# Kernel tuning notes

Hardware: AMD Instinct MI355X
Metric: run time of the kernel (lower is better)

The kernel has to match this reference:

```python
import jax, jax.numpy as jnp
import numpy as np


def _gcn_layer(x, W, b, src, dst, n_nodes):
    # PyG GCNConv: add self-loops, symmetric normalization, then
    # out[i] = sum_j norm_ij * (x[j] @ W) + b, norm_ij = deg_i^-1/2 * deg_j^-1/2
    h = x @ W  # [N, F_out]
    deg = jax.ops.segment_sum(jnp.ones_like(dst, dtype=h.dtype), dst, num_segments=n_nodes)
    dinv = jnp.where(deg > 0, jax.lax.rsqrt(deg), 0.0)
    norm = dinv[src] * dinv[dst]  # [E_total]
    msg = h[src] * norm[:, None]  # [E_total, F_out]
    out = jax.ops.segment_sum(msg, dst, num_segments=n_nodes)
    return out + b


def _add_self_loops(edge_index, n_nodes):
    loops = jnp.arange(n_nodes, dtype=edge_index.dtype)
    src = jnp.concatenate([edge_index[0], loops])
    dst = jnp.concatenate([edge_index[1], loops])
    return src, dst


def setup_inputs() -> dict:
    key = jax.random.key(0)
    ks = jax.random.split(key, 4)
    N, E, DIN, DOUT = 50000, 800000, 128, 64
    HID = 2 * DOUT
    x = jax.random.normal(ks[0], (N, DIN), dtype=jnp.float32)
    edge_index = jax.random.randint(ks[1], (2, E), 0, N, dtype=jnp.int64)
    W1 = jax.random.normal(ks[2], (DIN, HID), dtype=jnp.float32) / np.sqrt(DIN)
    b1 = jnp.zeros((HID,), dtype=jnp.float32)
    W2 = jax.random.normal(ks[3], (HID, DOUT), dtype=jnp.float32) / np.sqrt(HID)
    b2 = jnp.zeros((DOUT,), dtype=jnp.float32)
    return {"x": x, "edge_index": edge_index, "W1": W1, "b1": b1, "W2": W2, "b2": b2}


def reference(x, edge_index, W1, b1, W2, b2):
    n_nodes = x.shape[0]
    src, dst = _add_self_loops(edge_index, n_nodes)
    h = jax.nn.relu(_gcn_layer(x, W1, b1, src, dst, n_nodes))
    h = jax.nn.relu(_gcn_layer(h, W2, b2, src, dst, n_nodes))
    return h
```

## Files before the change

kernel.cpp:

```cpp
#include <hip/hip_runtime.h>

#define F_DIN  128
#define F_HID  128
#define F_DOUT 64
#define CAP    64
#define CNT_S  16

typedef __bf16 bf16x8 __attribute__((ext_vector_type(8)));
typedef float f32x4 __attribute__((ext_vector_type(4)));
typedef unsigned short ushort8 __attribute__((ext_vector_type(8)));
typedef unsigned short ushort4v __attribute__((ext_vector_type(4)));
typedef unsigned int uint4v __attribute__((ext_vector_type(4)));
typedef unsigned int uint2v __attribute__((ext_vector_type(2)));

static __device__ __forceinline__ unsigned short f2bf(float f) {
  unsigned u = __builtin_bit_cast(unsigned, f);
  u += 0x7FFF + ((u >> 16) & 1);
  return (unsigned short)(u >> 16);
}
static __device__ __forceinline__ float bflo(unsigned u) {
  return __builtin_bit_cast(float, u << 16);
}
static __device__ __forceinline__ float bfhi(unsigned u) {
  return __builtin_bit_cast(float, u & 0xFFFF0000u);
}


__global__ __launch_bounds__(256) void prep_zero(const float* __restrict__ W1,
                                                 const float* __restrict__ W2,
                                                 unsigned short* __restrict__ Wt1,
                                                 unsigned short* __restrict__ Wt2,
                                                 uint4v* __restrict__ zbase, int n16) {
  int i = blockIdx.x * 256 + threadIdx.x;
  if (i < n16) zbase[i] = uint4v{0u, 0u, 0u, 0u};
  if (i < F_HID * F_DIN) {
    int c = i / F_DIN, k = i % F_DIN;
    Wt1[i] = f2bf(W1[k * F_HID + c]);
  }
  int j = i - F_HID * F_DIN;
  if (j >= 0 && j < F_DOUT * F_HID) {
    int c = j / F_HID, k = j % F_HID;
    Wt2[j] = f2bf(W2[k * F_DOUT + c]);
  }
}


__global__ __launch_bounds__(256) void degfill_kernel(const int* __restrict__ src,
                                                      const int* __restrict__ dst,
                                                      int* __restrict__ cnt,
                                                      unsigned short* __restrict__ csr,
                                                      int E, int PS) {
  const int pid = (int)blockIdx.x & 7;
  const int lo = pid * PS;
  const int nch = gridDim.x >> 3;
  int i = ((int)blockIdx.x >> 3) * 256 + threadIdx.x;
  const int stride = nch * 256;
  for (; i < E; i += stride) {
    int d = dst[i];
    if ((unsigned)(d - lo) < (unsigned)PS) {
      int r = atomicAdd(&cnt[d * CNT_S], 1);
      if (r < CAP) csr[d * CAP + r] = (unsigned short)src[i];
    }
  }
}


template <int BN, bool AF32>
static __device__ __forceinline__ void gemm_body(const void* __restrict__ Ap,
                                                 const unsigned short* __restrict__ Wt,
                                                 unsigned short* __restrict__ Cout,
                                                 int M, int bid, int tid) {
  constexpr int K = 128;
  constexpr int NT = BN / 16;
  const int wv = tid >> 6;
  const int lane = tid & 63;
  const int r = lane & 15, g = lane >> 4;
  const int r0 = bid * 128 + wv * 32;

  f32x4 acc[2][NT];
#pragma unroll
  for (int t = 0; t < 2; ++t)
#pragma unroll
    for (int c = 0; c < NT; ++c) acc[t][c] = f32x4{0.f, 0.f, 0.f, 0.f};

#pragma unroll
  for (int kk = 0; kk < 4; ++kk) {
    const int kbase = kk * 32 + g * 8;
    bf16x8 afrag[2];
#pragma unroll
    for (int t = 0; t < 2; ++t) {
      int row = r0 + t * 16 + r;
      if (row >= M) row = M - 1;
      if (AF32) {
        const float* ap = (const float*)Ap + (size_t)row * K + kbase;
        float4 f0 = *(const float4*)(ap);
        float4 f1 = *(const float4*)(ap + 4);
        ushort8 h;
        h[0] = f2bf(f0.x); h[1] = f2bf(f0.y); h[2] = f2bf(f0.z); h[3] = f2bf(f0.w);
        h[4] = f2bf(f1.x); h[5] = f2bf(f1.y); h[6] = f2bf(f1.z); h[7] = f2bf(f1.w);
        afrag[t] = __builtin_bit_cast(bf16x8, h);
      } else {
        const unsigned short* ap = (const unsigned short*)Ap + (size_t)row * K + kbase;
        uint4v u = *(const uint4v*)ap;
        afrag[t] = __builtin_bit_cast(bf16x8, u);
      }
    }
#pragma unroll
    for (int c = 0; c < NT; ++c) {
      const int col = c * 16 + r;
      uint4v ub = *(const uint4v*)(Wt + (size_t)col * K + kbase);
      bf16x8 bfrag = __builtin_bit_cast(bf16x8, ub);
      acc[0][c] = __builtin_amdgcn_mfma_f32_16x16x32_bf16(afrag[0], bfrag, acc[0][c], 0, 0, 0);
      acc[1][c] = __builtin_amdgcn_mfma_f32_16x16x32_bf16(afrag[1], bfrag, acc[1][c], 0, 0, 0);
    }
  }

#pragma unroll
  for (int t = 0; t < 2; ++t)
#pragma unroll
    for (int c = 0; c < NT; ++c) {
      const int col = c * 16 + r;
#pragma unroll
      for (int j = 0; j < 4; ++j) {
        int row = r0 + t * 16 + g * 4 + j;
        if (row < M) Cout[(size_t)row * BN + col] = f2bf(acc[t][c][j]);
      }
    }
}

__global__ __launch_bounds__(256) void fat_gemm1_dinv(const float* __restrict__ x,
                                                      const unsigned short* __restrict__ Wt1,
                                                      unsigned short* __restrict__ H1, int M,
                                                      const int* __restrict__ cnt,
                                                      float* __restrict__ dinv,
                                                      int N, int gemmBlocks) {
  const int b = (int)blockIdx.x;
  if (b < gemmBlocks) {
    gemm_body<F_HID, true>(x, Wt1, H1, M, b, threadIdx.x);
  } else {
    int i = (b - gemmBlocks) * 256 + threadIdx.x;
    if (i < N) {
      int deg = cnt[i * CNT_S];
      dinv[i] = rsqrtf((float)(deg + 1));
    }
  }
}


__global__ __launch_bounds__(256, 8) void agg128_gemm2(const unsigned short* __restrict__ H,
                                                       const int* __restrict__ cnt,
                                                       const unsigned short* __restrict__ csr,
                                                       const float* __restrict__ dinv,
                                                       const float* __restrict__ bias,
                                                       const unsigned short* __restrict__ Wt2,
                                                       unsigned short* __restrict__ H2,
                                                       int Nn) {
  const int tid = threadIdx.x;
  const int lane = tid & 63;
  const int wv = tid >> 6;
  const int q = lane >> 4, ql = lane & 15;
  const int lrow = wv * 4 + q;
  const int node = blockIdx.x * 16 + lrow;

  __shared__ unsigned short ldsa[16 * 136];

  unsigned words[4] = {0u, 0u, 0u, 0u};
  if (node < Nn) {
    const float di = dinv[node];
    int deg = cnt[node * CNT_S];
    const int degc = deg < CAP ? deg : CAP;
    const uint4v us = *(const uint4v*)(H + (size_t)node * 128 + ql * 8);
    const unsigned short* slab = csr + (size_t)node * CAP;

    float acc[8];
#pragma unroll
    for (int i = 0; i < 8; ++i) acc[i] = 0.f;

    for (int f0 = 0; f0 < degc; f0 += 4) {
      ushort4v pk = *(const ushort4v*)(slab + f0);
      int sidx[4];
      float w[4];
#pragma unroll
      for (int j = 0; j < 4; ++j) {
        int s = (int)pk[j];
        sidx[j] = s < Nn ? s : Nn - 1;
        w[j] = (f0 + j < degc) ? dinv[sidx[j]] : 0.f;
      }
      uint4v u[4];
#pragma unroll
      for (int j = 0; j < 4; ++j)
        u[j] = *(const uint4v*)(H + (size_t)sidx[j] * 128 + ql * 8);
#pragma unroll
      for (int j = 0; j < 4; ++j)
#pragma unroll
        for (int i = 0; i < 4; ++i) {
          acc[2 * i]     = fmaf(w[j], bflo(u[j][i]), acc[2 * i]);
          acc[2 * i + 1] = fmaf(w[j], bfhi(u[j][i]), acc[2 * i + 1]);
        }
    }

    const float di2 = di * di;
#pragma unroll
    for (int i = 0; i < 4; ++i) {
      float v0 = di * acc[2 * i]     + di2 * bflo(us[i]) + bias[ql * 8 + 2 * i];
      float v1 = di * acc[2 * i + 1] + di2 * bfhi(us[i]) + bias[ql * 8 + 2 * i + 1];
      v0 = fmaxf(v0, 0.f); v1 = fmaxf(v1, 0.f);
      words[i] = (unsigned)f2bf(v0) | ((unsigned)f2bf(v1) << 16);
    }
  }
  {
    uint4v o; o[0] = words[0]; o[1] = words[1]; o[2] = words[2]; o[3] = words[3];
    *(uint4v*)(&ldsa[lrow * 136 + ql * 8]) = o;
  }
  __syncthreads();

  const int r = lane & 15, g = lane >> 4;
  f32x4 c = f32x4{0.f, 0.f, 0.f, 0.f};
#pragma unroll
  for (int kk = 0; kk < 4; ++kk) {
    const int kbase = kk * 32 + g * 8;
    bf16x8 a = __builtin_bit_cast(bf16x8, *(const uint4v*)(&ldsa[r * 136 + kbase]));
    bf16x8 b = __builtin_bit_cast(bf16x8, *(const uint4v*)(Wt2 + (size_t)(wv * 16 + r) * 128 + kbase));
    c = __builtin_amdgcn_mfma_f32_16x16x32_bf16(a, b, c, 0, 0, 0);
  }
#pragma unroll
  for (int j = 0; j < 4; ++j) {
    int no = blockIdx.x * 16 + g * 4 + j;
    if (no < Nn) H2[(size_t)no * 64 + wv * 16 + r] = f2bf(c[j]);
  }
}

__global__ __launch_bounds__(256, 8) void agg64_kernel(const unsigned short* __restrict__ H,
                                                       const int* __restrict__ cnt,
                                                       const unsigned short* __restrict__ csr,
                                                       const float* __restrict__ dinv,
                                                       const float* __restrict__ bias,
                                                       float* __restrict__ out,
                                                       int Nn) {
  const int lane = threadIdx.x & 63;
  const int wv = threadIdx.x >> 6;
  const int q = lane >> 4, ql = lane & 15;
  const int node = blockIdx.x * 16 + wv * 4 + q;
  if (node >= Nn) return;

  const float di = dinv[node];
  int deg = cnt[node * CNT_S];
  const int degc = deg < CAP ? deg : CAP;
  const uint2v us = *(const uint2v*)(H + (size_t)node * 64 + ql * 4);
  const unsigned short* slab = csr + (size_t)node * CAP;

  float acc[4];
#pragma unroll
  for (int i = 0; i < 4; ++i) acc[i] = 0.f;

  for (int f0 = 0; f0 < degc; f0 += 4) {
    ushort4v pk = *(const ushort4v*)(slab + f0);
    int sidx[4];
    float w[4];
#pragma unroll
    for (int j = 0; j < 4; ++j) {
      int s = (int)pk[j];
      sidx[j] = s < Nn ? s : Nn - 1;
      w[j] = (f0 + j < degc) ? dinv[sidx[j]] : 0.f;
    }
    uint2v u[4];
#pragma unroll
    for (int j = 0; j < 4; ++j)
      u[j] = *(const uint2v*)(H + (size_t)sidx[j] * 64 + ql * 4);
#pragma unroll
    for (int j = 0; j < 4; ++j)
#pragma unroll
      for (int i = 0; i < 2; ++i) {
        acc[2 * i]     = fmaf(w[j], bflo(u[j][i]), acc[2 * i]);
        acc[2 * i + 1] = fmaf(w[j], bfhi(u[j][i]), acc[2 * i + 1]);
      }
  }

  const float di2 = di * di;
  float4 o;
  o.x = fmaxf(di * acc[0] + di2 * bflo(us[0]) + bias[ql * 4 + 0], 0.f);
  o.y = fmaxf(di * acc[1] + di2 * bfhi(us[0]) + bias[ql * 4 + 1], 0.f);
  o.z = fmaxf(di * acc[2] + di2 * bflo(us[1]) + bias[ql * 4 + 2], 0.f);
  o.w = fmaxf(di * acc[3] + di2 * bfhi(us[1]) + bias[ql * 4 + 3], 0.f);
  *(float4*)(out + (size_t)node * 64 + ql * 4) = o;
}


extern "C" void kernel_launch(void* const* d_in, const int* in_sizes, int n_in,
                              void* d_out, int out_size, void* d_ws, size_t ws_size,
                              hipStream_t stream) {
  const float* x  = (const float*)d_in[0];
  const int*   ei = (const int*)d_in[1];
  const float* W1 = (const float*)d_in[2];
  const float* b1 = (const float*)d_in[3];
  const float* W2 = (const float*)d_in[4];
  const float* b2 = (const float*)d_in[5];
  float* out = (float*)d_out;

  const int E = in_sizes[1] / 2;
  const int N = in_sizes[0] / F_DIN;
  const int* src = ei;
  const int* dst = ei + E;

  char* ws = (char*)d_ws;
  auto alloc = [&](size_t bytes) {
    char* p = ws;
    ws += (bytes + 255) & ~(size_t)255;
    return p;
  };
  int*            cnt  = (int*)alloc((size_t)N * CNT_S * 4);
  float*          dinv = (float*)alloc((size_t)N * 4);
  unsigned short* csr  = (unsigned short*)alloc((size_t)N * CAP * 2);
  unsigned short* H1   = (unsigned short*)alloc((size_t)N * F_HID * 2);
  unsigned short* H2   = (unsigned short*)alloc((size_t)N * F_DOUT * 2);
  unsigned short* Wt1  = (unsigned short*)alloc((size_t)F_HID * F_DIN * 2);
  unsigned short* Wt2  = (unsigned short*)alloc((size_t)F_DOUT * F_HID * 2);

  const int gb = (N + 127) / 128;
  const int nb = (N + 255) / 256;
  const int PS = (N + 7) / 8;
  const int zero16 = (N * CNT_S * 4) / 16;
  int pgrid = (zero16 + 255) / 256;
  const int wgrid = (F_HID * F_DIN + F_DOUT * F_HID + 255) / 256;
  if (pgrid < wgrid) pgrid = wgrid;

  prep_zero<<<pgrid, 256, 0, stream>>>(W1, W2, Wt1, Wt2, (uint4v*)cnt, zero16);

  degfill_kernel<<<2048, 256, 0, stream>>>(src, dst, cnt, csr, E, PS);

  fat_gemm1_dinv<<<gb + nb, 256, 0, stream>>>(x, Wt1, H1, N, cnt, dinv, N, gb);

  agg128_gemm2<<<(N + 15) / 16, 256, 0, stream>>>(H1, cnt, csr, dinv, b1, Wt2, H2, N);

  agg64_kernel<<<(N + 15) / 16, 256, 0, stream>>>(H2, cnt, csr, dinv, b2, out, N);
}
```

Before: 114.6 us.

## Store hidden features in column-sliced layout and split aggregation by column block

GEMM1 now writes H1 as eight 16-column slabs (N×16 each), and GEMM2 writes H2 as eight 8-column slabs. The aggregation kernels run one column slab per block, interleaved across blocks, so each gathered row segment is small and the working set per slab (1.6 MB or 0.8 MB) can stay in cache. The fused agg128+gemm2 kernel is split into a standalone aggregation, an extra out1 buffer and a separate gemm2 launch. The cost is an extra kernel launch, an out1 round trip through memory, and rereading the CSR indices and dinv values once per column block.

```diff
diff --git a/kernel.cpp b/kernel.cpp
--- a/kernel.cpp
+++ b/kernel.cpp
@@ -65,11 +65,11 @@
 }
 
 
-template <int BN, bool AF32>
+template <int BN, int MODE>
 static __device__ __forceinline__ void gemm_body(const void* __restrict__ Ap,
                                                  const unsigned short* __restrict__ Wt,
                                                  unsigned short* __restrict__ Cout,
-                                                 int M, int bid, int tid) {
+                                                 int M, int Nn, int bid, int tid) {
   constexpr int K = 128;
   constexpr int NT = BN / 16;
   const int wv = tid >> 6;
@@ -91,7 +91,7 @@
     for (int t = 0; t < 2; ++t) {
       int row = r0 + t * 16 + r;
       if (row >= M) row = M - 1;
-      if (AF32) {
+      if (MODE == 0) {
         const float* ap = (const float*)Ap + (size_t)row * K + kbase;
         float4 f0 = *(const float4*)(ap);
         float4 f1 = *(const float4*)(ap + 4);
@@ -100,7 +100,8 @@
         h[4] = f2bf(f1.x); h[5] = f2bf(f1.y); h[6] = f2bf(f1.z); h[7] = f2bf(f1.w);
         afrag[t] = __builtin_bit_cast(bf16x8, h);
       } else {
-        const unsigned short* ap = (const unsigned short*)Ap + (size_t)row * K + kbase;
+        const unsigned short* ap = (const unsigned short*)Ap +
+            (size_t)(kk * 2 + (g >> 1)) * ((size_t)Nn * 16) + (size_t)row * 16 + (g & 1) * 8;
         uint4v u = *(const uint4v*)ap;
         afrag[t] = __builtin_bit_cast(bf16x8, u);
       }
@@ -123,7 +124,12 @@
 #pragma unroll
       for (int j = 0; j < 4; ++j) {
         int row = r0 + t * 16 + g * 4 + j;
-        if (row < M) Cout[(size_t)row * BN + col] = f2bf(acc[t][c][j]);
+        if (row < M) {
+          if (MODE == 0)
+            Cout[(size_t)c * ((size_t)Nn * 16) + (size_t)row * 16 + r] = f2bf(acc[t][c][j]);
+          else
+            Cout[(size_t)(col >> 3) * ((size_t)Nn * 8) + (size_t)row * 8 + (col & 7)] = f2bf(acc[t][c][j]);
+        }
       }
     }
 }
@@ -136,7 +142,7 @@
                                                       int N, int gemmBlocks) {
   const int b = (int)blockIdx.x;
   if (b < gemmBlocks) {
-    gemm_body<F_HID, true>(x, Wt1, H1, M, b, threadIdx.x);
+    gemm_body<F_HID, 0>(x, Wt1, H1, M, N, b, threadIdx.x);
   } else {
     int i = (b - gemmBlocks) * 256 + threadIdx.x;
     if (i < N) {
@@ -146,143 +152,119 @@
   }
 }
 
-
-__global__ __launch_bounds__(256, 8) void agg128_gemm2(const unsigned short* __restrict__ H,
-                                                       const int* __restrict__ cnt,
-                                                       const unsigned short* __restrict__ csr,
-                                                       const float* __restrict__ dinv,
-                                                       const float* __restrict__ bias,
-                                                       const unsigned short* __restrict__ Wt2,
-                                                       unsigned short* __restrict__ H2,
-                                                       int Nn) {
-  const int tid = threadIdx.x;
-  const int lane = tid & 63;
-  const int wv = tid >> 6;
-  const int q = lane >> 4, ql = lane & 15;
-  const int lrow = wv * 4 + q;
-  const int node = blockIdx.x * 16 + lrow;
-
-  __shared__ unsigned short ldsa[16 * 136];
-
-  unsigned words[4] = {0u, 0u, 0u, 0u};
-  if (node < Nn) {
-    const float di = dinv[node];
-    int deg = cnt[node * CNT_S];
-    const int degc = deg < CAP ? deg : CAP;
-    const uint4v us = *(const uint4v*)(H + (size_t)node * 128 + ql * 8);
-    const unsigned short* slab = csr + (size_t)node * CAP;
-
-    float acc[8];
-#pragma unroll
-    for (int i = 0; i < 8; ++i) acc[i] = 0.f;
-
-    for (int f0 = 0; f0 < degc; f0 += 4) {
-      ushort4v pk = *(const ushort4v*)(slab + f0);
-      int sidx[4];
-      float w[4];
-#pragma unroll
-      for (int j = 0; j < 4; ++j) {
-        int s = (int)pk[j];
-        sidx[j] = s < Nn ? s : Nn - 1;
-        w[j] = (f0 + j < degc) ? dinv[sidx[j]] : 0.f;
-      }
-      uint4v u[4];
-#pragma unroll
-      for (int j = 0; j < 4; ++j)
-        u[j] = *(const uint4v*)(H + (size_t)sidx[j] * 128 + ql * 8);
-#pragma unroll
-      for (int j = 0; j < 4; ++j)
-#pragma unroll
-        for (int i = 0; i < 4; ++i) {
-          acc[2 * i]     = fmaf(w[j], bflo(u[j][i]), acc[2 * i]);
-          acc[2 * i + 1] = fmaf(w[j], bfhi(u[j][i]), acc[2 * i + 1]);
-        }
-    }
-
-    const float di2 = di * di;
-#pragma unroll
-    for (int i = 0; i < 4; ++i) {
-      float v0 = di * acc[2 * i]     + di2 * bflo(us[i]) + bias[ql * 8 + 2 * i];
-      float v1 = di * acc[2 * i + 1] + di2 * bfhi(us[i]) + bias[ql * 8 + 2 * i + 1];
-      v0 = fmaxf(v0, 0.f); v1 = fmaxf(v1, 0.f);
-      words[i] = (unsigned)f2bf(v0) | ((unsigned)f2bf(v1) << 16);
-    }
-  }
-  {
-    uint4v o; o[0] = words[0]; o[1] = words[1]; o[2] = words[2]; o[3] = words[3];
-    *(uint4v*)(&ldsa[lrow * 136 + ql * 8]) = o;
-  }
-  __syncthreads();
-
-  const int r = lane & 15, g = lane >> 4;
-  f32x4 c = f32x4{0.f, 0.f, 0.f, 0.f};
-#pragma unroll
-  for (int kk = 0; kk < 4; ++kk) {
-    const int kbase = kk * 32 + g * 8;
-    bf16x8 a = __builtin_bit_cast(bf16x8, *(const uint4v*)(&ldsa[r * 136 + kbase]));
-    bf16x8 b = __builtin_bit_cast(bf16x8, *(const uint4v*)(Wt2 + (size_t)(wv * 16 + r) * 128 + kbase));
-    c = __builtin_amdgcn_mfma_f32_16x16x32_bf16(a, b, c, 0, 0, 0);
-  }
-#pragma unroll
-  for (int j = 0; j < 4; ++j) {
-    int no = blockIdx.x * 16 + g * 4 + j;
-    if (no < Nn) H2[(size_t)no * 64 + wv * 16 + r] = f2bf(c[j]);
-  }
-}
-
-__global__ __launch_bounds__(256, 8) void agg64_kernel(const unsigned short* __restrict__ H,
-                                                       const int* __restrict__ cnt,
-                                                       const unsigned short* __restrict__ csr,
-                                                       const float* __restrict__ dinv,
-                                                       const float* __restrict__ bias,
-                                                       float* __restrict__ out,
-                                                       int Nn) {
-  const int lane = threadIdx.x & 63;
-  const int wv = threadIdx.x >> 6;
-  const int q = lane >> 4, ql = lane & 15;
-  const int node = blockIdx.x * 16 + wv * 4 + q;
+__global__ __launch_bounds__(256) void gemm2_kernel(const unsigned short* __restrict__ out1,
+                                                    const unsigned short* __restrict__ Wt2,
+                                                    unsigned short* __restrict__ H2,
+                                                    int M, int N) {
+  gemm_body<F_DOUT, 1>(out1, Wt2, H2, M, N, blockIdx.x, threadIdx.x);
+}
+
+
+__global__ __launch_bounds__(256) void agg128_cs(const unsigned short* __restrict__ H,
+                                                 const int* __restrict__ cnt,
+                                                 const unsigned short* __restrict__ csr,
+                                                 const float* __restrict__ dinv,
+                                                 const float* __restrict__ bias,
+                                                 unsigned short* __restrict__ out1,
+                                                 int Nn) {
+  const int cb = (int)blockIdx.x & 7;
+  const int grp = threadIdx.x >> 2;
+  const int l = threadIdx.x & 3;
+  const int node = ((int)blockIdx.x >> 3) * 64 + grp;
   if (node >= Nn) return;
 
+  const unsigned short* Hs = H + (size_t)cb * ((size_t)Nn * 16);
   const float di = dinv[node];
   int deg = cnt[node * CNT_S];
   const int degc = deg < CAP ? deg : CAP;
-  const uint2v us = *(const uint2v*)(H + (size_t)node * 64 + ql * 4);
   const unsigned short* slab = csr + (size_t)node * CAP;
-
-  float acc[4];
-#pragma unroll
-  for (int i = 0; i < 4; ++i) acc[i] = 0.f;
-
+  const uint2v us = *(const uint2v*)(Hs + (size_t)node * 16 + l * 4);
+
+  float acc[4] = {0.f, 0.f, 0.f, 0.f};
   for (int f0 = 0; f0 < degc; f0 += 4) {
     ushort4v pk = *(const ushort4v*)(slab + f0);
-    int sidx[4];
+    int s[4];
     float w[4];
 #pragma unroll
     for (int j = 0; j < 4; ++j) {
-      int s = (int)pk[j];
-      sidx[j] = s < Nn ? s : Nn - 1;
-      w[j] = (f0 + j < degc) ? dinv[sidx[j]] : 0.f;
+      int si = (int)pk[j];
+      s[j] = si < Nn ? si : Nn - 1;
+      w[j] = (f0 + j < degc) ? dinv[s[j]] : 0.f;
     }
     uint2v u[4];
 #pragma unroll
     for (int j = 0; j < 4; ++j)
-      u[j] = *(const uint2v*)(H + (size_t)sidx[j] * 64 + ql * 4);
+      u[j] = *(const uint2v*)(Hs + (size_t)s[j] * 16 + l * 4);
+#pragma unroll
+    for (int j = 0; j < 4; ++j) {
+      acc[0] = fmaf(w[j], bflo(u[j][0]), acc[0]);
+      acc[1] = fmaf(w[j], bfhi(u[j][0]), acc[1]);
+      acc[2] = fmaf(w[j], bflo(u[j][1]), acc[2]);
+      acc[3] = fmaf(w[j], bfhi(u[j][1]), acc[3]);
+    }
+  }
+
+  const float di2 = di * di;
+  const int colb = cb * 16 + l * 4;
+  float v0 = fmaxf(di * acc[0] + di2 * bflo(us[0]) + bias[colb + 0], 0.f);
+  float v1 = fmaxf(di * acc[1] + di2 * bfhi(us[0]) + bias[colb + 1], 0.f);
+  float v2 = fmaxf(di * acc[2] + di2 * bflo(us[1]) + bias[colb + 2], 0.f);
+  float v3 = fmaxf(di * acc[3] + di2 * bfhi(us[1]) + bias[colb + 3], 0.f);
+  uint2v o;
+  o[0] = (unsigned)f2bf(v0) | ((unsigned)f2bf(v1) << 16);
+  o[1] = (unsigned)f2bf(v2) | ((unsigned)f2bf(v3) << 16);
+  *(uint2v*)(out1 + (size_t)cb * ((size_t)Nn * 16) + (size_t)node * 16 + l * 4) = o;
+}
+
+
+__global__ __launch_bounds__(256) void agg64_cs(const unsigned short* __restrict__ H,
+                                                const int* __restrict__ cnt,
+                                                const unsigned short* __restrict__ csr,
+                                                const float* __restrict__ dinv,
+                                                const float* __restrict__ bias,
+                                                float* __restrict__ out,
+                                                int Nn) {
+  const int cb = (int)blockIdx.x & 7;
+  const int grp = threadIdx.x >> 2;
+  const int l = threadIdx.x & 3;
+  const int node = ((int)blockIdx.x >> 3) * 64 + grp;
+  if (node >= Nn) return;
+
+  const unsigned short* Hs = H + (size_t)cb * ((size_t)Nn * 8);
+  const float di = dinv[node];
+  int deg = cnt[node * CNT_S];
+  const int degc = deg < CAP ? deg : CAP;
+  const unsigned short* slab = csr + (size_t)node * CAP;
+  const unsigned us = *(const unsigned*)(Hs + (size_t)node * 8 + l * 2);
+
+  float acc[2] = {0.f, 0.f};
+  for (int f0 = 0; f0 < degc; f0 += 4) {
+    ushort4v pk = *(const ushort4v*)(slab + f0);
+    int s[4];
+    float w[4];
+#pragma unroll
+    for (int j = 0; j < 4; ++j) {
+      int si = (int)pk[j];
+      s[j] = si < Nn ? si : Nn - 1;
+      w[j] = (f0 + j < degc) ? dinv[s[j]] : 0.f;
+    }
+    unsigned u[4];
 #pragma unroll
     for (int j = 0; j < 4; ++j)
-#pragma unroll
-      for (int i = 0; i < 2; ++i) {
-        acc[2 * i]     = fmaf(w[j], bflo(u[j][i]), acc[2 * i]);
-        acc[2 * i + 1] = fmaf(w[j], bfhi(u[j][i]), acc[2 * i + 1]);
-      }
+      u[j] = *(const unsigned*)(Hs + (size_t)s[j] * 8 + l * 2);
+#pragma unroll
+    for (int j = 0; j < 4; ++j) {
+      acc[0] = fmaf(w[j], bflo(u[j]), acc[0]);
+      acc[1] = fmaf(w[j], bfhi(u[j]), acc[1]);
+    }
   }
 
   const float di2 = di * di;
-  float4 o;
-  o.x = fmaxf(di * acc[0] + di2 * bflo(us[0]) + bias[ql * 4 + 0], 0.f);
-  o.y = fmaxf(di * acc[1] + di2 * bfhi(us[0]) + bias[ql * 4 + 1], 0.f);
-  o.z = fmaxf(di * acc[2] + di2 * bflo(us[1]) + bias[ql * 4 + 2], 0.f);
-  o.w = fmaxf(di * acc[3] + di2 * bfhi(us[1]) + bias[ql * 4 + 3], 0.f);
-  *(float4*)(out + (size_t)node * 64 + ql * 4) = o;
+  const int colb = cb * 8 + l * 2;
+  float2 o;
+  o.x = fmaxf(di * acc[0] + di2 * bflo(us) + bias[colb + 0], 0.f);
+  o.y = fmaxf(di * acc[1] + di2 * bfhi(us) + bias[colb + 1], 0.f);
+  *(float2*)(out + (size_t)node * 64 + colb) = o;
 }
 
 
@@ -312,6 +294,7 @@
   float*          dinv = (float*)alloc((size_t)N * 4);
   unsigned short* csr  = (unsigned short*)alloc((size_t)N * CAP * 2);
   unsigned short* H1   = (unsigned short*)alloc((size_t)N * F_HID * 2);
+  unsigned short* out1 = (unsigned short*)alloc((size_t)N * F_HID * 2);
   unsigned short* H2   = (unsigned short*)alloc((size_t)N * F_DOUT * 2);
   unsigned short* Wt1  = (unsigned short*)alloc((size_t)F_HID * F_DIN * 2);
   unsigned short* Wt2  = (unsigned short*)alloc((size_t)F_DOUT * F_HID * 2);
@@ -319,6 +302,7 @@
   const int gb = (N + 127) / 128;
   const int nb = (N + 255) / 256;
   const int PS = (N + 7) / 8;
+  const int ab = ((N + 63) / 64) * 8;
   const int zero16 = (N * CNT_S * 4) / 16;
   int pgrid = (zero16 + 255) / 256;
   const int wgrid = (F_HID * F_DIN + F_DOUT * F_HID + 255) / 256;
@@ -330,7 +314,9 @@
 
   fat_gemm1_dinv<<<gb + nb, 256, 0, stream>>>(x, Wt1, H1, N, cnt, dinv, N, gb);
 
-  agg128_gemm2<<<(N + 15) / 16, 256, 0, stream>>>(H1, cnt, csr, dinv, b1, Wt2, H2, N);
-
-  agg64_kernel<<<(N + 15) / 16, 256, 0, stream>>>(H2, cnt, csr, dinv, b2, out, N);
-}
+  agg128_cs<<<ab, 256, 0, stream>>>(H1, cnt, csr, dinv, b1, out1, N);
+
+  gemm2_kernel<<<gb, 256, 0, stream>>>(out1, Wt2, H2, N, N);
+
+  agg64_cs<<<ab, 256, 0, stream>>>(H2, cnt, csr, dinv, b2, out, N);
+}
```

New measurement: 196.3 us. 71.2% more time.
